# Optimization experiments

Measured on AMD Instinct MI355X. Metric: run time of the kernel, lower is better.

## Reference

```python
import jax, jax.numpy as jnp
import numpy as np

B, S, H = 8, 2048, 256

def setup_inputs() -> dict:
    key = jax.random.key(0)
    ks = jax.random.split(key, 7)
    sc = 0.05
    return {
        "inputs": jax.random.normal(ks[0], (B, S, H), dtype=jnp.float32),
        "Wq": jax.random.normal(ks[1], (H, H), dtype=jnp.float32) * sc,
        "bq": jax.random.normal(ks[2], (H,), dtype=jnp.float32) * sc,
        "Wk": jax.random.normal(ks[3], (H, H), dtype=jnp.float32) * sc,
        "bk": jax.random.normal(ks[4], (H,), dtype=jnp.float32) * sc,
        "Wv": jax.random.normal(ks[5], (H, H), dtype=jnp.float32) * sc,
        "bv": jax.random.normal(ks[6], (H,), dtype=jnp.float32) * sc,
    }

def reference(inputs, Wq, bq, Wk, bk, Wv, bv):
    # nn.Linear: y = x @ W.T + b
    q = jnp.einsum("bsh,oh->bso", inputs, Wq) + bq
    k = jnp.einsum("bsh,oh->bso", inputs, Wk) + bk
    v = jnp.einsum("bsh,oh->bso", inputs, Wv) + bv
    hidden = q.shape[-1]
    # NOTE: original scales by sqrt(hidden^2) == hidden (not sqrt(hidden))
    scores = jnp.einsum("bqh,bkh->bqk", q, k) / jnp.float32(hidden)
    # NOTE: original applies softmax over dim=1 (the query axis), not the last axis
    weights = jax.nn.softmax(scores, axis=1)
    return jnp.einsum("bqk,bkh->bqh", weights, v)
```

## Files before the change

### kernel.cpp

```cpp
#include <hip/hip_runtime.h>
#include <hip/hip_bf16.h>

#define B_ 8
#define S_ 2048
#define H_ 256
#define BS_ (B_*S_)

typedef __attribute__((ext_vector_type(8))) short bf16x8;
typedef __attribute__((ext_vector_type(4))) short bf16x4;
typedef __attribute__((ext_vector_type(4))) float f32x4;

static __device__ inline short f2bf(float f) {
  union { float f; unsigned int u; } a; a.f = f;
  unsigned int u = a.u;
  unsigned int r = (u + 0x7fffu + ((u >> 16) & 1u)) >> 16;
  return (short)r;
}

static __device__ inline float bf2f(short s) {
  union { float f; unsigned int u; } a;
  a.u = ((unsigned int)(unsigned short)s) << 16;
  return a.f;
}

static __device__ inline f32x4 mfma16(bf16x8 a, bf16x8 b, f32x4 c) {
  return __builtin_amdgcn_mfma_f32_16x16x32_bf16(a, b, c, 0, 0, 0);
}

static __device__ inline void gl_lds16(const short* g, short* l) {
  __builtin_amdgcn_global_load_lds(
      (const __attribute__((address_space(1))) void*)g,
      (__attribute__((address_space(3))) void*)l, 16, 0, 0);
}

#define NX4 (BS_ * H_ / 4)
#define NW4 (H_ * H_ / 4)
#define NTOT4 (NX4 + 3 * NW4)

__global__ __launch_bounds__(256) void cvt_bf16(
    const float* __restrict__ x,
    const float* __restrict__ Wq, const float* __restrict__ Wk,
    const float* __restrict__ Wv,
    short* __restrict__ xb, short* __restrict__ wqb,
    short* __restrict__ wkb, short* __restrict__ wvb)
{
  int stride = gridDim.x * blockDim.x;
  for (int i = blockIdx.x * blockDim.x + threadIdx.x; i < NTOT4; i += stride) {
    const float* src; short* dst; int off;
    if (i < NX4) { src = x; dst = xb; off = i; }
    else {
      int j = i - NX4;
      int w = j >> 14;
      off = j & (NW4 - 1);
      src = (w == 0) ? Wq : (w == 1) ? Wk : Wv;
      dst = (w == 0) ? wqb : (w == 1) ? wkb : wvb;
    }
    float4 v = *(const float4*)(src + off * 4);
    bf16x4 p;
    p[0] = f2bf(v.x); p[1] = f2bf(v.y); p[2] = f2bf(v.z); p[3] = f2bf(v.w);
    *(bf16x4*)(dst + off * 4) = p;
  }
}

__global__ __launch_bounds__(256) void qkv_proj(
    const short* __restrict__ x,
    const short* __restrict__ Wq, const float* __restrict__ bq,
    const short* __restrict__ Wk, const float* __restrict__ bk,
    const short* __restrict__ Wv, const float* __restrict__ bv,
    short* __restrict__ Qo, short* __restrict__ Ko, short* __restrict__ VTo)
{
  const int tid  = threadIdx.x;
  const int wave = tid >> 6;
  const int lane = tid & 63;
  const int quad = lane >> 4;
  const int l16  = lane & 15;
  const int y    = blockIdx.y;

  const short* W    = (y == 0) ? Wq : (y == 1) ? Wk : Wv;
  const float* bias = (y == 0) ? bq : (y == 1) ? bk : bv;
  const int sblk = blockIdx.x * 64;
  const int s0   = sblk + wave * 16;

  __shared__ short wbuf[16 * 512];
  __shared__ short xbuf[4 * 512];

  f32x4 zero = {0.f, 0.f, 0.f, 0.f};
  f32x4 acc[16];
#pragma unroll
  for (int i = 0; i < 16; i++) acc[i] = zero;

  for (int ch = 0; ch < 8; ch++) {
#pragma unroll
    for (int i = 0; i < 4; i++) {
      int r = wave * 4 + i;
      gl_lds16(W + (r * 16 + l16) * H_ + ch * 32 + quad * 8, wbuf + r * 512);
    }
    gl_lds16(x + (s0 + l16) * H_ + ch * 32 + quad * 8, xbuf + wave * 512);
    __syncthreads();
    bf16x8 a = *(const bf16x8*)(xbuf + wave * 512 + lane * 8);
#pragma unroll
    for (int nf = 0; nf < 16; nf++) {
      bf16x8 bb = *(const bf16x8*)(wbuf + nf * 512 + lane * 8);
      acc[nf] = mfma16(a, bb, acc[nf]);
    }
    __syncthreads();
  }

  if (y < 2) {
    short* dst = (y == 0) ? Qo : Ko;
#pragma unroll
    for (int nf = 0; nf < 16; nf++) {
      int col = nf * 16 + l16;
      float bvl = bias[col];
#pragma unroll
      for (int r = 0; r < 4; r++) {
        int row = s0 + quad * 4 + r;
        dst[row * H_ + col] = f2bf(acc[nf][r] + bvl);
      }
    }
  } else {
    int row0  = s0 + quad * 4;
    int b_idx = row0 >> 11;
    int k0    = row0 & (S_ - 1);
#pragma unroll
    for (int nf = 0; nf < 16; nf++) {
      int col = nf * 16 + l16;
      float bvl = bias[col];
      bf16x4 pk;
#pragma unroll
      for (int r = 0; r < 4; r++) pk[r] = f2bf(acc[nf][r] + bvl);
      *(bf16x4*)(VTo + (size_t)b_idx * H_ * S_ + (size_t)col * S_ + k0) = pk;
    }
  }
}

__global__ __launch_bounds__(256) void zero_den(float* __restrict__ den)
{
  int i = blockIdx.x * 256 + threadIdx.x;
  if (i < BS_) den[i] = 0.f;
}

__global__ __launch_bounds__(256) void scores(
    const short* __restrict__ Q, const short* __restrict__ K,
    short* __restrict__ Pf, float* __restrict__ den)
{
  const int tid  = threadIdx.x;
  const int wave = tid >> 6;
  const int lane = tid & 63;
  const int quad = lane >> 4;
  const int l16  = lane & 15;
  const int qt = blockIdx.x & 15;
  const int kt = (blockIdx.x >> 4) & 15;
  const int b  = blockIdx.x >> 8;

  const short* Qb = Q + b * S_ * H_;
  const short* Kb = K + b * S_ * H_;

  const int krow0 = kt * 128 + wave * 32;
  const int qcol0 = qt * 128;
  const int kw    = krow0 >> 5;

  __shared__ short kbuf[8 * 512];
  __shared__ short qbuf[8 * 512];

  f32x4 zero = {0.f, 0.f, 0.f, 0.f};
  f32x4 acc[2][8];
#pragma unroll
  for (int i = 0; i < 2; i++)
#pragma unroll
    for (int j = 0; j < 8; j++) acc[i][j] = zero;

  for (int ch = 0; ch < 8; ch++) {
#pragma unroll
    for (int i = 0; i < 2; i++) {
      int r = wave * 2 + i;
      gl_lds16(Kb + (kt * 128 + r * 16 + l16) * H_ + ch * 32 + quad * 8,
               kbuf + r * 512);
      gl_lds16(Qb + (qcol0 + r * 16 + l16) * H_ + ch * 32 + quad * 8,
               qbuf + r * 512);
    }
    __syncthreads();
    bf16x8 a0 = *(const bf16x8*)(kbuf + (wave * 2 + 0) * 512 + lane * 8);
    bf16x8 a1 = *(const bf16x8*)(kbuf + (wave * 2 + 1) * 512 + lane * 8);
#pragma unroll
    for (int qf = 0; qf < 8; qf++) {
      bf16x8 bq = *(const bf16x8*)(qbuf + qf * 512 + lane * 8);
      acc[0][qf] = mfma16(a0, bq, acc[0][qf]);
      acc[1][qf] = mfma16(a1, bq, acc[1][qf]);
    }
    __syncthreads();
  }

  const int quadA = quad >> 1;
  const int j0    = (quad & 1) * 4;
  float rs[2][4] = {{0.f,0.f,0.f,0.f},{0.f,0.f,0.f,0.f}};
#pragma unroll
  for (int kf = 0; kf < 2; kf++) {
#pragma unroll
    for (int qf = 0; qf < 8; qf++) {
      bf16x4 pk;
#pragma unroll
      for (int r = 0; r < 4; r++) {
        float e = __expf(acc[kf][qf][r] * (1.0f / H_));
        rs[kf][r] += e;
        pk[r] = f2bf(e);
      }
      size_t tile = ((size_t)(b * 128 + qt * 8 + qf) << 6) + kw;
      *(bf16x4*)(Pf + (tile << 9) + ((2 * kf + quadA) * 16 + l16) * 8 + j0) = pk;
    }
  }

#pragma unroll
  for (int kf = 0; kf < 2; kf++) {
#pragma unroll
    for (int r = 0; r < 4; r++) {
      float v = rs[kf][r];
      v += __shfl_xor(v, 1, 64);
      v += __shfl_xor(v, 2, 64);
      v += __shfl_xor(v, 4, 64);
      v += __shfl_xor(v, 8, 64);
      if (l16 == 0)
        atomicAdd(&den[b * S_ + krow0 + kf * 16 + quad * 4 + r], v);
    }
  }
}

__global__ __launch_bounds__(256) void den_rcp(
    const float* __restrict__ den, float* __restrict__ rcp)
{
  int i = blockIdx.x * 256 + threadIdx.x;
  if (i < BS_) rcp[i] = 1.0f / den[i];
}

__global__ __launch_bounds__(256) void vscale(
    short* __restrict__ VT, const float* __restrict__ rcp)
{
  int i = blockIdx.x * 256 + threadIdx.x;
  int b  = i >> 17;
  int k0 = (i & 511) << 2;
  float4 rf = *(const float4*)(rcp + b * S_ + k0);
  bf16x4 v = *(bf16x4*)(VT + (size_t)i * 4);
  bf16x4 o;
  o[0] = f2bf(bf2f(v[0]) * rf.x);
  o[1] = f2bf(bf2f(v[1]) * rf.y);
  o[2] = f2bf(bf2f(v[2]) * rf.z);
  o[3] = f2bf(bf2f(v[3]) * rf.w);
  *(bf16x4*)(VT + (size_t)i * 4) = o;
}

__global__ __launch_bounds__(256) void pv(
    const short* __restrict__ Pf, const short* __restrict__ VTs,
    float* __restrict__ out)
{
  const int tid  = threadIdx.x;
  const int wave = tid >> 6;
  const int lane = tid & 63;
  const int quad = lane >> 4;
  const int l16  = lane & 15;
  const int bx = blockIdx.x;
  const int qt = bx >> 4;
  const int b  = (bx >> 1) & 7;
  const int hs = bx & 1;

  __shared__ short vbuf[16 * 512];
  __shared__ short abuf[8 * 512];

  const int qt16 = qt * 4 + wave;
  const short* VTb = VTs + (size_t)b * H_ * S_ + (size_t)(hs * 128) * S_;
  const size_t tilebase = ((size_t)(b * 128 + qt16) * 64) << 9;

  f32x4 zero = {0.f, 0.f, 0.f, 0.f};
  f32x4 acc[8];
#pragma unroll
  for (int i = 0; i < 8; i++) acc[i] = zero;

  for (int kc = 0; kc < S_; kc += 64) {
#pragma unroll
    for (int i = 0; i < 4; i++) {
      int id = wave * 4 + i;
      int n  = id >> 1;
      int kw = id & 1;
      const short* g = VTb + (size_t)(n * 16 + l16) * S_ + kc + kw * 32 + quad * 8;
      gl_lds16(g, vbuf + id * 512);
    }
#pragma unroll
    for (int kwi = 0; kwi < 2; kwi++) {
      const short* g = Pf + tilebase + (size_t)((kc >> 5) + kwi) * 512 + lane * 8;
      gl_lds16(g, abuf + (wave * 2 + kwi) * 512);
    }
    __syncthreads();
#pragma unroll
    for (int kw = 0; kw < 2; kw++) {
      bf16x8 a = *(const bf16x8*)(abuf + (wave * 2 + kw) * 512 + lane * 8);
#pragma unroll
      for (int n = 0; n < 8; n++) {
        bf16x8 vb = *(const bf16x8*)(vbuf + (n * 2 + kw) * 512 + lane * 8);
        acc[n] = mfma16(a, vb, acc[n]);
      }
    }
    __syncthreads();
  }

  const int q0 = qt16 * 16;
#pragma unroll
  for (int n = 0; n < 8; n++) {
    int col = hs * 128 + n * 16 + l16;
#pragma unroll
    for (int r = 0; r < 4; r++) {
      int q = q0 + quad * 4 + r;
      out[((size_t)b * S_ + q) * H_ + col] = acc[n][r];
    }
  }
}

extern "C" void kernel_launch(void* const* d_in, const int* in_sizes, int n_in,
                              void* d_out, int out_size, void* d_ws, size_t ws_size,
                              hipStream_t stream) {
  const float* x  = (const float*)d_in[0];
  const float* Wq = (const float*)d_in[1];
  const float* bq = (const float*)d_in[2];
  const float* Wk = (const float*)d_in[3];
  const float* bk = (const float*)d_in[4];
  const float* Wv = (const float*)d_in[5];
  const float* bv = (const float*)d_in[6];

  short* xb  = (short*)d_ws;
  short* wqb = xb  + (size_t)BS_ * H_;
  short* wkb = wqb + H_ * H_;
  short* wvb = wkb + H_ * H_;
  short* Qs  = wvb + H_ * H_;
  short* Ks  = Qs  + (size_t)BS_ * H_;
  short* VT  = Ks  + (size_t)BS_ * H_;
  short* P   = VT  + (size_t)BS_ * H_;
  float* den = (float*)(P + (size_t)B_ * S_ * S_);
  float* rcp = den + BS_;
  float* outp = (float*)d_out;

  cvt_bf16<<<1024, 256, 0, stream>>>(x, Wq, Wk, Wv, xb, wqb, wkb, wvb);
  qkv_proj<<<dim3(BS_ / 64, 3), 256, 0, stream>>>(xb, wqb, bq, wkb, bk, wvb, bv, Qs, Ks, VT);
  zero_den<<<64, 256, 0, stream>>>(den);
  scores<<<2048, 256, 0, stream>>>(Qs, Ks, P, den);
  den_rcp<<<64, 256, 0, stream>>>(den, rcp);
  vscale<<<4096, 256, 0, stream>>>(VT, rcp);
  pv<<<512, 256, 0, stream>>>(P, VT, outp);
}
```

Before: 198.2 us.

## Enlarge scores K tile, re-split qkv_proj by output column, fold small kernels

The scores kernel now covers 256 key rows per block instead of 128, so each Q tile loaded into LDS is reused across more MFMAs, and the grid halves. qkv_proj now gives each wave four output-column fragments across all four 16-row strips instead of all 16 columns for one strip, which changes A/B fragment reuse from LDS. The zero_den and den_rcp launches are removed: den is zeroed inside the conversion kernel and vscale divides by den directly. This cuts launch count and LDS traffic, but the larger scores tile raises register pressure (32 accumulators) and may lower occupancy.

```diff
diff --git a/kernel.cpp b/kernel.cpp
--- a/kernel.cpp
+++ b/kernel.cpp
@@ -36,16 +36,23 @@
 #define NX4 (BS_ * H_ / 4)
 #define NW4 (H_ * H_ / 4)
 #define NTOT4 (NX4 + 3 * NW4)
+#define NALL4 (NTOT4 + BS_ / 4)
 
 __global__ __launch_bounds__(256) void cvt_bf16(
     const float* __restrict__ x,
     const float* __restrict__ Wq, const float* __restrict__ Wk,
     const float* __restrict__ Wv,
     short* __restrict__ xb, short* __restrict__ wqb,
-    short* __restrict__ wkb, short* __restrict__ wvb)
+    short* __restrict__ wkb, short* __restrict__ wvb,
+    float* __restrict__ den)
 {
   int stride = gridDim.x * blockDim.x;
-  for (int i = blockIdx.x * blockDim.x + threadIdx.x; i < NTOT4; i += stride) {
+  for (int i = blockIdx.x * blockDim.x + threadIdx.x; i < NALL4; i += stride) {
+    if (i >= NTOT4) {
+      float4 z = {0.f, 0.f, 0.f, 0.f};
+      *(float4*)(den + (size_t)(i - NTOT4) * 4) = z;
+      continue;
+    }
     const float* src; short* dst; int off;
     if (i < NX4) { src = x; dst = xb; off = i; }
     else {
@@ -79,15 +86,16 @@
   const short* W    = (y == 0) ? Wq : (y == 1) ? Wk : Wv;
   const float* bias = (y == 0) ? bq : (y == 1) ? bk : bv;
   const int sblk = blockIdx.x * 64;
-  const int s0   = sblk + wave * 16;
 
   __shared__ short wbuf[16 * 512];
   __shared__ short xbuf[4 * 512];
 
   f32x4 zero = {0.f, 0.f, 0.f, 0.f};
-  f32x4 acc[16];
-#pragma unroll
-  for (int i = 0; i < 16; i++) acc[i] = zero;
+  f32x4 acc[4][4];
+#pragma unroll
+  for (int i = 0; i < 4; i++)
+#pragma unroll
+    for (int j = 0; j < 4; j++) acc[i][j] = zero;
 
   for (int ch = 0; ch < 8; ch++) {
 #pragma unroll
@@ -95,13 +103,19 @@
       int r = wave * 4 + i;
       gl_lds16(W + (r * 16 + l16) * H_ + ch * 32 + quad * 8, wbuf + r * 512);
     }
-    gl_lds16(x + (s0 + l16) * H_ + ch * 32 + quad * 8, xbuf + wave * 512);
-    __syncthreads();
-    bf16x8 a = *(const bf16x8*)(xbuf + wave * 512 + lane * 8);
-#pragma unroll
-    for (int nf = 0; nf < 16; nf++) {
-      bf16x8 bb = *(const bf16x8*)(wbuf + nf * 512 + lane * 8);
-      acc[nf] = mfma16(a, bb, acc[nf]);
+    gl_lds16(x + (sblk + wave * 16 + l16) * H_ + ch * 32 + quad * 8,
+             xbuf + wave * 512);
+    __syncthreads();
+    bf16x8 af[4];
+#pragma unroll
+    for (int st = 0; st < 4; st++)
+      af[st] = *(const bf16x8*)(xbuf + st * 512 + lane * 8);
+#pragma unroll
+    for (int i = 0; i < 4; i++) {
+      bf16x8 bb = *(const bf16x8*)(wbuf + (wave * 4 + i) * 512 + lane * 8);
+#pragma unroll
+      for (int st = 0; st < 4; st++)
+        acc[st][i] = mfma16(af[st], bb, acc[st][i]);
     }
     __syncthreads();
   }
@@ -109,35 +123,35 @@
   if (y < 2) {
     short* dst = (y == 0) ? Qo : Ko;
 #pragma unroll
-    for (int nf = 0; nf < 16; nf++) {
-      int col = nf * 16 + l16;
+    for (int i = 0; i < 4; i++) {
+      int col = (wave * 4 + i) * 16 + l16;
       float bvl = bias[col];
 #pragma unroll
-      for (int r = 0; r < 4; r++) {
-        int row = s0 + quad * 4 + r;
-        dst[row * H_ + col] = f2bf(acc[nf][r] + bvl);
+      for (int st = 0; st < 4; st++) {
+#pragma unroll
+        for (int r = 0; r < 4; r++) {
+          int row = sblk + st * 16 + quad * 4 + r;
+          dst[row * H_ + col] = f2bf(acc[st][i][r] + bvl);
+        }
       }
     }
   } else {
-    int row0  = s0 + quad * 4;
-    int b_idx = row0 >> 11;
-    int k0    = row0 & (S_ - 1);
-#pragma unroll
-    for (int nf = 0; nf < 16; nf++) {
-      int col = nf * 16 + l16;
+#pragma unroll
+    for (int i = 0; i < 4; i++) {
+      int col = (wave * 4 + i) * 16 + l16;
       float bvl = bias[col];
-      bf16x4 pk;
-#pragma unroll
-      for (int r = 0; r < 4; r++) pk[r] = f2bf(acc[nf][r] + bvl);
-      *(bf16x4*)(VTo + (size_t)b_idx * H_ * S_ + (size_t)col * S_ + k0) = pk;
-    }
-  }
-}
-
-__global__ __launch_bounds__(256) void zero_den(float* __restrict__ den)
-{
-  int i = blockIdx.x * 256 + threadIdx.x;
-  if (i < BS_) den[i] = 0.f;
+#pragma unroll
+      for (int st = 0; st < 4; st++) {
+        int row0  = sblk + st * 16 + quad * 4;
+        int b_idx = row0 >> 11;
+        int k0    = row0 & (S_ - 1);
+        bf16x4 pk;
+#pragma unroll
+        for (int r = 0; r < 4; r++) pk[r] = f2bf(acc[st][i][r] + bvl);
+        *(bf16x4*)(VTo + (size_t)b_idx * H_ * S_ + (size_t)col * S_ + k0) = pk;
+      }
+    }
+  }
 }
 
 __global__ __launch_bounds__(256) void scores(
@@ -150,52 +164,59 @@
   const int quad = lane >> 4;
   const int l16  = lane & 15;
   const int qt = blockIdx.x & 15;
-  const int kt = (blockIdx.x >> 4) & 15;
-  const int b  = blockIdx.x >> 8;
+  const int kt = (blockIdx.x >> 4) & 7;
+  const int b  = blockIdx.x >> 7;
 
   const short* Qb = Q + b * S_ * H_;
   const short* Kb = K + b * S_ * H_;
 
-  const int krow0 = kt * 128 + wave * 32;
+  const int krow0 = kt * 256 + wave * 64;
   const int qcol0 = qt * 128;
-  const int kw    = krow0 >> 5;
-
-  __shared__ short kbuf[8 * 512];
+
+  __shared__ short kbuf[16 * 512];
   __shared__ short qbuf[8 * 512];
 
   f32x4 zero = {0.f, 0.f, 0.f, 0.f};
-  f32x4 acc[2][8];
-#pragma unroll
-  for (int i = 0; i < 2; i++)
+  f32x4 acc[4][8];
+#pragma unroll
+  for (int i = 0; i < 4; i++)
 #pragma unroll
     for (int j = 0; j < 8; j++) acc[i][j] = zero;
 
   for (int ch = 0; ch < 8; ch++) {
+#pragma unroll
+    for (int i = 0; i < 4; i++) {
+      int r = wave * 4 + i;
+      gl_lds16(Kb + (kt * 256 + r * 16 + l16) * H_ + ch * 32 + quad * 8,
+               kbuf + r * 512);
+    }
 #pragma unroll
     for (int i = 0; i < 2; i++) {
       int r = wave * 2 + i;
-      gl_lds16(Kb + (kt * 128 + r * 16 + l16) * H_ + ch * 32 + quad * 8,
-               kbuf + r * 512);
       gl_lds16(Qb + (qcol0 + r * 16 + l16) * H_ + ch * 32 + quad * 8,
                qbuf + r * 512);
     }
     __syncthreads();
-    bf16x8 a0 = *(const bf16x8*)(kbuf + (wave * 2 + 0) * 512 + lane * 8);
-    bf16x8 a1 = *(const bf16x8*)(kbuf + (wave * 2 + 1) * 512 + lane * 8);
+    bf16x8 af[4];
+#pragma unroll
+    for (int i = 0; i < 4; i++)
+      af[i] = *(const bf16x8*)(kbuf + (wave * 4 + i) * 512 + lane * 8);
 #pragma unroll
     for (int qf = 0; qf < 8; qf++) {
       bf16x8 bq = *(const bf16x8*)(qbuf + qf * 512 + lane * 8);
-      acc[0][qf] = mfma16(a0, bq, acc[0][qf]);
-      acc[1][qf] = mfma16(a1, bq, acc[1][qf]);
-    }
-    __syncthreads();
-  }
-
-  const int quadA = quad >> 1;
-  const int j0    = (quad & 1) * 4;
-  float rs[2][4] = {{0.f,0.f,0.f,0.f},{0.f,0.f,0.f,0.f}};
-#pragma unroll
-  for (int kf = 0; kf < 2; kf++) {
+#pragma unroll
+      for (int i = 0; i < 4; i++)
+        acc[i][qf] = mfma16(af[i], bq, acc[i][qf]);
+    }
+    __syncthreads();
+  }
+
+  const int j0 = (quad & 1) * 4;
+  float rs[4][4] = {{0,0,0,0},{0,0,0,0},{0,0,0,0},{0,0,0,0}};
+#pragma unroll
+  for (int kf = 0; kf < 4; kf++) {
+    int kw    = kt * 8 + wave * 2 + (kf >> 1);
+    int quadA = 2 * (kf & 1) + (quad >> 1);
 #pragma unroll
     for (int qf = 0; qf < 8; qf++) {
       bf16x4 pk;
@@ -206,12 +227,12 @@
         pk[r] = f2bf(e);
       }
       size_t tile = ((size_t)(b * 128 + qt * 8 + qf) << 6) + kw;
-      *(bf16x4*)(Pf + (tile << 9) + ((2 * kf + quadA) * 16 + l16) * 8 + j0) = pk;
-    }
-  }
-
-#pragma unroll
-  for (int kf = 0; kf < 2; kf++) {
+      *(bf16x4*)(Pf + (tile << 9) + (quadA * 16 + l16) * 8 + j0) = pk;
+    }
+  }
+
+#pragma unroll
+  for (int kf = 0; kf < 4; kf++) {
 #pragma unroll
     for (int r = 0; r < 4; r++) {
       float v = rs[kf][r];
@@ -225,26 +246,19 @@
   }
 }
 
-__global__ __launch_bounds__(256) void den_rcp(
-    const float* __restrict__ den, float* __restrict__ rcp)
-{
-  int i = blockIdx.x * 256 + threadIdx.x;
-  if (i < BS_) rcp[i] = 1.0f / den[i];
-}
-
 __global__ __launch_bounds__(256) void vscale(
-    short* __restrict__ VT, const float* __restrict__ rcp)
+    short* __restrict__ VT, const float* __restrict__ den)
 {
   int i = blockIdx.x * 256 + threadIdx.x;
   int b  = i >> 17;
   int k0 = (i & 511) << 2;
-  float4 rf = *(const float4*)(rcp + b * S_ + k0);
+  float4 df = *(const float4*)(den + b * S_ + k0);
   bf16x4 v = *(bf16x4*)(VT + (size_t)i * 4);
   bf16x4 o;
-  o[0] = f2bf(bf2f(v[0]) * rf.x);
-  o[1] = f2bf(bf2f(v[1]) * rf.y);
-  o[2] = f2bf(bf2f(v[2]) * rf.z);
-  o[3] = f2bf(bf2f(v[3]) * rf.w);
+  o[0] = f2bf(bf2f(v[0]) / df.x);
+  o[1] = f2bf(bf2f(v[1]) / df.y);
+  o[2] = f2bf(bf2f(v[2]) / df.z);
+  o[3] = f2bf(bf2f(v[3]) / df.w);
   *(bf16x4*)(VT + (size_t)i * 4) = o;
 }
 
@@ -333,14 +347,11 @@
   short* VT  = Ks  + (size_t)BS_ * H_;
   short* P   = VT  + (size_t)BS_ * H_;
   float* den = (float*)(P + (size_t)B_ * S_ * S_);
-  float* rcp = den + BS_;
   float* outp = (float*)d_out;
 
-  cvt_bf16<<<1024, 256, 0, stream>>>(x, Wq, Wk, Wv, xb, wqb, wkb, wvb);
+  cvt_bf16<<<1024, 256, 0, stream>>>(x, Wq, Wk, Wv, xb, wqb, wkb, wvb, den);
   qkv_proj<<<dim3(BS_ / 64, 3), 256, 0, stream>>>(xb, wqb, bq, wkb, bk, wvb, bv, Qs, Ks, VT);
-  zero_den<<<64, 256, 0, stream>>>(den);
-  scores<<<2048, 256, 0, stream>>>(Qs, Ks, P, den);
-  den_rcp<<<64, 256, 0, stream>>>(den, rcp);
-  vscale<<<4096, 256, 0, stream>>>(VT, rcp);
+  scores<<<1024, 256, 0, stream>>>(Qs, Ks, P, den);
+  vscale<<<4096, 256, 0, stream>>>(VT, den);
   pv<<<512, 256, 0, stream>>>(P, VT, outp);
 }
```

After: 214.0 us. +8.0%, slower.
